# Kernel optimization log

Measured on AMD Instinct MI355X. Metric: run time of the kernel, lower is better.

Reference implementation:

```python
import jax, jax.numpy as jnp
import numpy as np

VOCAB = 100000; E = 256; H = 256; Hh = 128; K = 12
START = 9; STOP = 10; PAD = 11; NEG = -10000.0
B = 32; T = 512


def setup_inputs() -> dict:
    key = jax.random.key(0)
    ks = jax.random.split(key, 16)
    u = 1.0 / np.sqrt(Hh)  # pytorch LSTM init scale
    xav = lambda k, shape: jax.random.normal(k, shape, jnp.float32) * np.sqrt(2.0 / (shape[0] + shape[1]))
    trans = jax.random.normal(ks[10], (K, K), jnp.float32)
    trans = trans.at[START, :].set(NEG).at[:, STOP].set(NEG)
    trans = trans.at[PAD, :].set(NEG).at[:, PAD].set(NEG)
    return {
        "sentence": jax.random.randint(ks[0], (B, T), 0, VOCAB),
        "h0": jax.random.normal(ks[1], (2, B, Hh), jnp.float32),
        "c0": jax.random.normal(ks[2], (2, B, Hh), jnp.float32),
        "embed": xav(ks[3], (VOCAB, E)),
        "W_ih_f": jax.random.uniform(ks[4], (4 * Hh, E), jnp.float32, -u, u),
        "W_hh_f": jax.random.uniform(ks[5], (4 * Hh, Hh), jnp.float32, -u, u),
        "b_f": jax.random.uniform(ks[6], (4 * Hh,), jnp.float32, -u, u),
        "W_ih_r": jax.random.uniform(ks[7], (4 * Hh, E), jnp.float32, -u, u),
        "W_hh_r": jax.random.uniform(ks[8], (4 * Hh, Hh), jnp.float32, -u, u),
        "b_r": jax.random.uniform(ks[9], (4 * Hh,), jnp.float32, -u, u),
        "W_out": xav(ks[11], (K, H)),
        "b_out": jnp.zeros((K,), jnp.float32),
        "transitions": trans,
    }


def _lstm_dir(xe, W_ih, W_hh, b, h0, c0):
    # xe: [T,B,E]; precompute input contribution once (big GEMM outside scan)
    xg = jnp.einsum('tbe,ge->tbg', xe, W_ih) + b  # [T,B,4*Hh]
    def step(carry, xt):
        h, c = carry
        g = xt + h @ W_hh.T
        i, f, gg, o = jnp.split(g, 4, axis=-1)  # pytorch gate order i,f,g,o
        c = jax.nn.sigmoid(f) * c + jax.nn.sigmoid(i) * jnp.tanh(gg)
        h = jax.nn.sigmoid(o) * jnp.tanh(c)
        return (h, c), h
    _, hs = jax.lax.scan(step, (h0, c0), xg)
    return hs  # [T,B,Hh]


def reference(sentence, h0, c0, embed, W_ih_f, W_hh_f, b_f, W_ih_r, W_hh_r, b_r,
              W_out, b_out, transitions):
    xe = embed[sentence].transpose(1, 0, 2)  # [T,B,E]
    hs_f = _lstm_dir(xe, W_ih_f, W_hh_f, b_f, h0[0], c0[0])
    hs_r = _lstm_dir(xe[::-1], W_ih_r, W_hh_r, b_r, h0[1], c0[1])[::-1]
    hs = jnp.concatenate([hs_f, hs_r], axis=-1)           # [T,B,H]
    feats = hs @ W_out.T + b_out                          # [T,B,K]

    # Viterbi max-plus recurrence
    scores0 = jnp.full((B, K), NEG, jnp.float32).at[:, START].set(0.0)
    def vstep(scores, feat):
        m = scores[:, None, :] + transitions[None, :, :]  # [B,K_next,K_prev]
        ptr = jnp.argmax(m, axis=-1).astype(jnp.int32)
        return jnp.max(m, axis=-1) + feat, ptr
    scores, pointers = jax.lax.scan(vstep, scores0, feats)  # pointers [T,B,K]
    scores = scores + transitions[STOP]
    best_tag = jnp.argmax(scores, axis=-1).astype(jnp.int32)  # [B]

    # parallel backtrace (reverse scan, outputs in original time order)
    def back(tag, ptr):
        prev = jnp.take_along_axis(ptr, tag[:, None], axis=1)[:, 0]
        return prev, tag
    _, path = jax.lax.scan(back, best_tag, pointers, reverse=True)  # [T,B]
    return path.T  # [B,T] int32 best tag sequence
```

## Files before the change

### kernel.cpp

```cpp
#include <hip/hip_runtime.h>
#include <hip/hip_bf16.h>
#include <cmath>

#define TT 512
#define BB 32
#define EE 256
#define HH 128
#define KCRF 12
#define NEGF (-10000.0f)

__global__ __launch_bounds__(256) void k1_xg(const int* __restrict__ sent,
    const float* __restrict__ embed,
    const float* __restrict__ Wf, const float* __restrict__ bf,
    const float* __restrict__ Wr, const float* __restrict__ br,
    float* __restrict__ XG)
{
  __shared__ __align__(16) float As[64][36];
  __shared__ __align__(16) float Bs[128][36];
  const int tid = threadIdx.x;
  const int m0 = (blockIdx.x >> 3) * 64;
  const int n0 = (blockIdx.x & 7) * 128;
  const int ty = tid >> 4, tx = tid & 15;
  float acc[4][8];
#pragma unroll
  for (int i = 0; i < 4; ++i)
#pragma unroll
    for (int j = 0; j < 8; ++j) acc[i][j] = 0.f;

  for (int k0 = 0; k0 < 256; k0 += 32) {
#pragma unroll
    for (int r = 0; r < 2; ++r) {
      int idx = tid + r * 256;
      int row = idx >> 3;
      int c4 = (idx & 7) << 2;
      int R = m0 + row;
      int t = R >> 5, b = R & 31;
      const float4 v = *(const float4*)(embed + (long)sent[b * TT + t] * 256 + k0 + c4);
      *(float4*)&As[row][c4] = v;
    }
#pragma unroll
    for (int r = 0; r < 4; ++r) {
      int idx = tid + r * 256;
      int row = idx >> 3;
      int c4 = (idx & 7) << 2;
      int col = n0 + row;
      const float* src = (col < 512) ? (Wf + (long)col * 256) : (Wr + (long)(col - 512) * 256);
      const float4 v = *(const float4*)(src + k0 + c4);
      *(float4*)&Bs[row][c4] = v;
    }
    __syncthreads();
#pragma unroll
    for (int kk = 0; kk < 32; ++kk) {
      float a[4], bv[8];
#pragma unroll
      for (int i = 0; i < 4; ++i) a[i] = As[ty * 4 + i][kk];
#pragma unroll
      for (int j = 0; j < 8; ++j) bv[j] = Bs[tx + 16 * j][kk];
#pragma unroll
      for (int i = 0; i < 4; ++i)
#pragma unroll
        for (int j = 0; j < 8; ++j) acc[i][j] = fmaf(a[i], bv[j], acc[i][j]);
    }
    __syncthreads();
  }
#pragma unroll
  for (int i = 0; i < 4; ++i) {
    int R = m0 + ty * 4 + i;
#pragma unroll
    for (int j = 0; j < 8; ++j) {
      int col = n0 + tx + 16 * j;
      float bias = (col < 512) ? bf[col] : br[col - 512];
      XG[(long)R * 1024 + col] = acc[i][j] + bias;
    }
  }
}

__global__ __launch_bounds__(512) __attribute__((amdgpu_waves_per_eu(1)))
void k2_scan(const float* __restrict__ XG,
    const float* __restrict__ Whf, const float* __restrict__ Whr,
    const float* __restrict__ h0, const float* __restrict__ c0,
    float* __restrict__ HS)
{
  const int wg = blockIdx.x;
  const int dir = wg >> 5;
  const int b = wg & 31;
  const int j = threadIdx.x;
  const float* Wh = dir ? Whr : Whf;

  float4 w[32];
#pragma unroll
  for (int i = 0; i < 32; ++i)
    w[i] = *(const float4*)(Wh + (long)j * 128 + i * 4);

  __shared__ __align__(16) float hs[128];
  __shared__ float gs[512];
  float c = 0.f;
  if (j < 128) {
    hs[j] = h0[(dir * 32 + b) * 128 + j];
    c = c0[(dir * 32 + b) * 128 + j];
  }
  __syncthreads();

  const int t0 = dir ? (TT - 1) : 0;
  const long stepoff = dir ? -32768 : 32768;
  const float* xp = XG + ((long)t0 * 32 + b) * 1024 + dir * 512 + j;
  float xg_cur = *xp;
  const int gate = j >> 7;

  for (int s = 0; s < TT; ++s) {
    const int t = dir ? (TT - 1 - s) : s;
    float xg_nxt = 0.f;
    if (s + 1 < TT) { xp += stepoff; xg_nxt = *xp; }

    float a0 = xg_cur, a1 = 0.f, a2 = 0.f, a3 = 0.f;
#pragma unroll
    for (int i = 0; i < 32; ++i) {
      const float4 hv = *(const float4*)(hs + 4 * i);
      a0 = fmaf(w[i].x, hv.x, a0);
      a1 = fmaf(w[i].y, hv.y, a1);
      a2 = fmaf(w[i].z, hv.z, a2);
      a3 = fmaf(w[i].w, hv.w, a3);
    }
    const float acc = (a0 + a1) + (a2 + a3);
    const float act = (gate == 2) ? tanhf(acc) : (1.f / (1.f + expf(-acc)));
    gs[j] = act;
    __syncthreads();
    if (j < 128) {
      float ig = gs[j], fg = gs[128 + j], gg = gs[256 + j], og = gs[384 + j];
      c = fmaf(fg, c, ig * gg);
      float h = og * tanhf(c);
      hs[j] = h;
      HS[((long)t * 32 + b) * 256 + dir * 128 + j] = h;
    }
    __syncthreads();
    xg_cur = xg_nxt;
  }
}

__global__ __launch_bounds__(64) void k3_feats(const float* __restrict__ HS,
    const float* __restrict__ Wout, const float* __restrict__ bout,
    float* __restrict__ FE)
{
  __shared__ __align__(16) float ws[12 * 256];
  __shared__ float bs[12];
  const int tid = threadIdx.x;
  for (int i = tid; i < 768; i += 64)
    ((float4*)ws)[i] = ((const float4*)Wout)[i];
  if (tid < 12) bs[tid] = bout[tid];
  __syncthreads();
  const long row = (long)blockIdx.x * 64 + tid;
  const float4* hp = (const float4*)(HS + row * 256);
  float acc[12];
#pragma unroll
  for (int k = 0; k < 12; ++k) acc[k] = bs[k];
  for (int e4 = 0; e4 < 64; ++e4) {
    float4 hv = hp[e4];
#pragma unroll
    for (int k = 0; k < 12; ++k) {
      const float4 wv = *(const float4*)&ws[k * 256 + e4 * 4];
      acc[k] = fmaf(hv.x, wv.x, acc[k]);
      acc[k] = fmaf(hv.y, wv.y, acc[k]);
      acc[k] = fmaf(hv.z, wv.z, acc[k]);
      acc[k] = fmaf(hv.w, wv.w, acc[k]);
    }
  }
  const int t = (int)(row >> 5), b = (int)(row & 31);
#pragma unroll
  for (int k = 0; k < 12; ++k) FE[((long)t * 12 + k) * 32 + b] = acc[k];
}

__global__ __launch_bounds__(64) void k4_viterbi(const float* __restrict__ FE,
    const float* __restrict__ trans, int* __restrict__ out)
{
  __shared__ unsigned char ptrl[TT * 48];
  __shared__ __align__(16) float sc[2][4][12];
  const int l = threadIdx.x;
  const int bsub = l / 12;
  const int nxt = l % 12;
  const bool act = (bsub < 4);
  const int bs = act ? bsub : 0;
  const int b = blockIdx.x * 4 + bs;

  float tr[12], stopv[12];
#pragma unroll
  for (int p = 0; p < 12; ++p) tr[p] = trans[nxt * 12 + p];
#pragma unroll
  for (int p = 0; p < 12; ++p) stopv[p] = trans[10 * 12 + p];

  if (act) sc[0][bsub][nxt] = (nxt == 9) ? 0.f : NEGF;
  __syncthreads();

  float fnext = FE[nxt * 32 + b];
  for (int t = 0; t < TT; ++t) {
    const int cur = t & 1;
    const float feat = fnext;
    if (t + 1 < TT) fnext = FE[((t + 1) * 12 + nxt) * 32 + b];

    float sp[12];
    *(float4*)&sp[0] = *(const float4*)&sc[cur][bs][0];
    *(float4*)&sp[4] = *(const float4*)&sc[cur][bs][4];
    *(float4*)&sp[8] = *(const float4*)&sc[cur][bs][8];
    float best = -1e30f; int arg = 0;
#pragma unroll
    for (int p = 0; p < 12; ++p) {
      const float v = sp[p] + tr[p];
      if (v > best) { best = v; arg = p; }
    }
    if (act) {
      sc[cur ^ 1][bsub][nxt] = best + feat;
      ptrl[t * 48 + bsub * 12 + nxt] = (unsigned char)arg;
    }
    __syncthreads();
    }

  float best = -1e30f; int arg = 0;
#pragma unroll
  for (int p = 0; p < 12; ++p) {
    const float v = sc[0][bs][p] + stopv[p];
    if (v > best) { best = v; arg = p; }
  }
  if (act && nxt == 0) {
    int tag = arg;
    for (int t = TT - 1; t >= 0; --t) {
      out[b * TT + t] = tag;
      if (t) tag = ptrl[t * 48 + bsub * 12 + tag];
    }
  }
}

extern "C" void kernel_launch(void* const* d_in, const int* in_sizes, int n_in,
                              void* d_out, int out_size, void* d_ws, size_t ws_size,
                              hipStream_t stream)
{
  const int* sent = (const int*)d_in[0];
  const float* h0 = (const float*)d_in[1];
  const float* c0 = (const float*)d_in[2];
  const float* embed = (const float*)d_in[3];
  const float* Wif = (const float*)d_in[4];
  const float* Whf = (const float*)d_in[5];
  const float* bf = (const float*)d_in[6];
  const float* Wir = (const float*)d_in[7];
  const float* Whr = (const float*)d_in[8];
  const float* br = (const float*)d_in[9];
  const float* Wout = (const float*)d_in[10];
  const float* bout = (const float*)d_in[11];
  const float* trans = (const float*)d_in[12];

  char* ws = (char*)d_ws;
  float* XG = (float*)ws;
  float* HS = (float*)(ws + 67108864);
  float* FE = (float*)(ws + 67108864 + 16777216);
  int* out = (int*)d_out;

  hipLaunchKernelGGL(k1_xg, dim3(2048), dim3(256), 0, stream,
                     sent, embed, Wif, bf, Wir, br, XG);
  hipLaunchKernelGGL(k2_scan, dim3(64), dim3(512), 0, stream,
                     XG, Whf, Whr, h0, c0, HS);
  hipLaunchKernelGGL(k3_feats, dim3(256), dim3(64), 0, stream,
                     HS, Wout, bout, FE);
  hipLaunchKernelGGL(k4_viterbi, dim3(8), dim3(64), 0, stream,
                     FE, trans, out);
}
```

Measured before the change: 780.4 us.

## Fuse input-projection GEMM with LSTM scan using flag-based producer/consumer overlap

Merges the input-gate GEMM and the recurrent LSTM scan into one persistent kernel. 64 blocks run the scan while 192 blocks compute XG tiles in time order, outward from both ends so the forward and reverse directions are fed. The producers signal completion through atomic flags, and the scan blocks poll these flags every 16 steps. The goal is to hide the GEMM behind the serial scan, at the cost of requiring all blocks to be co-resident, a memset, and spin-wait overhead.

```diff
diff --git a/kernel.cpp b/kernel.cpp
--- a/kernel.cpp
+++ b/kernel.cpp
@@ -9,131 +9,154 @@
 #define KCRF 12
 #define NEGF (-10000.0f)
 
-__global__ __launch_bounds__(256) void k1_xg(const int* __restrict__ sent,
-    const float* __restrict__ embed,
-    const float* __restrict__ Wf, const float* __restrict__ bf,
-    const float* __restrict__ Wr, const float* __restrict__ br,
-    float* __restrict__ XG)
+__global__ __launch_bounds__(512)
+void k12_fused(const int* __restrict__ sent, const float* __restrict__ embed,
+               const float* __restrict__ Wf, const float* __restrict__ bfv,
+               const float* __restrict__ Wr, const float* __restrict__ brv,
+               const float* __restrict__ Whf, const float* __restrict__ Whr,
+               const float* __restrict__ h0, const float* __restrict__ c0,
+               float* XG, float* __restrict__ HS, int* flags)
 {
   __shared__ __align__(16) float As[64][36];
-  __shared__ __align__(16) float Bs[128][36];
-  const int tid = threadIdx.x;
-  const int m0 = (blockIdx.x >> 3) * 64;
-  const int n0 = (blockIdx.x & 7) * 128;
-  const int ty = tid >> 4, tx = tid & 15;
-  float acc[4][8];
-#pragma unroll
-  for (int i = 0; i < 4; ++i)
-#pragma unroll
-    for (int j = 0; j < 8; ++j) acc[i][j] = 0.f;
-
-  for (int k0 = 0; k0 < 256; k0 += 32) {
-#pragma unroll
-    for (int r = 0; r < 2; ++r) {
-      int idx = tid + r * 256;
-      int row = idx >> 3;
-      int c4 = (idx & 7) << 2;
-      int R = m0 + row;
-      int t = R >> 5, b = R & 31;
-      const float4 v = *(const float4*)(embed + (long)sent[b * TT + t] * 256 + k0 + c4);
-      *(float4*)&As[row][c4] = v;
-    }
-#pragma unroll
-    for (int r = 0; r < 4; ++r) {
-      int idx = tid + r * 256;
-      int row = idx >> 3;
-      int c4 = (idx & 7) << 2;
-      int col = n0 + row;
-      const float* src = (col < 512) ? (Wf + (long)col * 256) : (Wr + (long)(col - 512) * 256);
-      const float4 v = *(const float4*)(src + k0 + c4);
-      *(float4*)&Bs[row][c4] = v;
-    }
-    __syncthreads();
-#pragma unroll
-    for (int kk = 0; kk < 32; ++kk) {
-      float a[4], bv[8];
-#pragma unroll
-      for (int i = 0; i < 4; ++i) a[i] = As[ty * 4 + i][kk];
-#pragma unroll
-      for (int j = 0; j < 8; ++j) bv[j] = Bs[tx + 16 * j][kk];
-#pragma unroll
-      for (int i = 0; i < 4; ++i)
-#pragma unroll
-        for (int j = 0; j < 8; ++j) acc[i][j] = fmaf(a[i], bv[j], acc[i][j]);
-    }
-    __syncthreads();
-  }
-#pragma unroll
-  for (int i = 0; i < 4; ++i) {
-    int R = m0 + ty * 4 + i;
-#pragma unroll
-    for (int j = 0; j < 8; ++j) {
-      int col = n0 + tx + 16 * j;
-      float bias = (col < 512) ? bf[col] : br[col - 512];
-      XG[(long)R * 1024 + col] = acc[i][j] + bias;
-    }
-  }
-}
-
-__global__ __launch_bounds__(512) __attribute__((amdgpu_waves_per_eu(1)))
-void k2_scan(const float* __restrict__ XG,
-    const float* __restrict__ Whf, const float* __restrict__ Whr,
-    const float* __restrict__ h0, const float* __restrict__ c0,
-    float* __restrict__ HS)
-{
-  const int wg = blockIdx.x;
-  const int dir = wg >> 5;
-  const int b = wg & 31;
-  const int j = threadIdx.x;
-  const float* Wh = dir ? Whr : Whf;
-
-  float4 w[32];
-#pragma unroll
-  for (int i = 0; i < 32; ++i)
-    w[i] = *(const float4*)(Wh + (long)j * 128 + i * 4);
-
+  __shared__ __align__(16) float Bs[256][36];
   __shared__ __align__(16) float hs[128];
   __shared__ float gs[512];
-  float c = 0.f;
-  if (j < 128) {
-    hs[j] = h0[(dir * 32 + b) * 128 + j];
-    c = c0[(dir * 32 + b) * 128 + j];
-  }
-  __syncthreads();
-
-  const int t0 = dir ? (TT - 1) : 0;
-  const long stepoff = dir ? -32768 : 32768;
-  const float* xp = XG + ((long)t0 * 32 + b) * 1024 + dir * 512 + j;
-  float xg_cur = *xp;
-  const int gate = j >> 7;
-
-  for (int s = 0; s < TT; ++s) {
-    const int t = dir ? (TT - 1 - s) : s;
-    float xg_nxt = 0.f;
-    if (s + 1 < TT) { xp += stepoff; xg_nxt = *xp; }
-
-    float a0 = xg_cur, a1 = 0.f, a2 = 0.f, a3 = 0.f;
-#pragma unroll
-    for (int i = 0; i < 32; ++i) {
-      const float4 hv = *(const float4*)(hs + 4 * i);
-      a0 = fmaf(w[i].x, hv.x, a0);
-      a1 = fmaf(w[i].y, hv.y, a1);
-      a2 = fmaf(w[i].z, hv.z, a2);
-      a3 = fmaf(w[i].w, hv.w, a3);
-    }
-    const float acc = (a0 + a1) + (a2 + a3);
-    const float act = (gate == 2) ? tanhf(acc) : (1.f / (1.f + expf(-acc)));
-    gs[j] = act;
+
+  const int wg = blockIdx.x;
+  const int tid = threadIdx.x;
+
+  if (wg >= 64) {
+    const int sub = tid >> 8;
+    const int t256 = tid & 255;
+    const int ty = t256 >> 4, tx = t256 & 15;
+    for (int item = wg - 64; item < 1024; item += 192) {
+      const int g = item >> 2, q = item & 3;
+      const int pair = (q < 2) ? g : (255 - g);
+      const int half = q >> 1;
+      const int n0 = (q & 1) * 256 + half * 512;
+      const int m0 = pair * 64;
+      const int colbase = n0 + sub * 128;
+
+      float acc[4][8];
+#pragma unroll
+      for (int i = 0; i < 4; ++i)
+#pragma unroll
+        for (int j = 0; j < 8; ++j) acc[i][j] = 0.f;
+
+      for (int k0 = 0; k0 < 256; k0 += 32) {
+        {
+          int row = tid >> 3, c4 = (tid & 7) << 2;
+          int R = m0 + row, t = R >> 5, b = R & 31;
+          *(float4*)&As[row][c4] =
+              *(const float4*)(embed + (long)sent[b * TT + t] * 256 + k0 + c4);
+        }
+#pragma unroll
+        for (int r = 0; r < 4; ++r) {
+          int idx = tid + r * 512, row = idx >> 3, c4 = (idx & 7) << 2;
+          int col = n0 + row;
+          const float* src = (col < 512) ? (Wf + (long)col * 256)
+                                         : (Wr + (long)(col - 512) * 256);
+          *(float4*)&Bs[row][c4] = *(const float4*)(src + k0 + c4);
+        }
+        __syncthreads();
+#pragma unroll
+        for (int kk = 0; kk < 32; ++kk) {
+          float a[4], bv[8];
+#pragma unroll
+          for (int i = 0; i < 4; ++i) a[i] = As[ty * 4 + i][kk];
+#pragma unroll
+          for (int j = 0; j < 8; ++j) bv[j] = Bs[sub * 128 + tx + 16 * j][kk];
+#pragma unroll
+          for (int i = 0; i < 4; ++i)
+#pragma unroll
+            for (int j = 0; j < 8; ++j) acc[i][j] = fmaf(a[i], bv[j], acc[i][j]);
+        }
+        __syncthreads();
+      }
+#pragma unroll
+      for (int i = 0; i < 4; ++i) {
+        const long R = m0 + ty * 4 + i;
+#pragma unroll
+        for (int j = 0; j < 8; ++j) {
+          const int col = colbase + tx + 16 * j;
+          const float bias = (col < 512) ? bfv[col] : brv[col - 512];
+          XG[R * 1024 + col] = acc[i][j] + bias;
+        }
+      }
+      __syncthreads();
+      if (tid == 0) { __threadfence(); atomicAdd(&flags[pair * 2 + half], 1); }
+    }
+  } else {
+    const int dir = wg >> 5;
+    const int b = wg & 31;
+    const int j = tid;
+    const float* Wh = dir ? Whr : Whf;
+
+    float4 w[32];
+#pragma unroll
+    for (int i = 0; i < 32; ++i)
+      w[i] = *(const float4*)(Wh + (long)j * 128 + i * 4);
+
+    float c = 0.f;
+    if (j < 128) {
+      hs[j] = h0[(dir * 32 + b) * 128 + j];
+      c = c0[(dir * 32 + b) * 128 + j];
+    }
     __syncthreads();
-    if (j < 128) {
-      float ig = gs[j], fg = gs[128 + j], gg = gs[256 + j], og = gs[384 + j];
-      c = fmaf(fg, c, ig * gg);
-      float h = og * tanhf(c);
-      hs[j] = h;
-      HS[((long)t * 32 + b) * 256 + dir * 128 + j] = h;
-    }
-    __syncthreads();
-    xg_cur = xg_nxt;
+
+    const int t0 = dir ? (TT - 1) : 0;
+    const long stepoff = dir ? -32768 : 32768;
+    const float* xp = XG + ((long)t0 * 32 + b) * 1024 + dir * 512 + j;
+    const int gate = j >> 7;
+
+    {
+      if (tid < 9) {
+        int p0 = dir ? ((TT - 1) >> 1) : 0;
+        int p = dir ? (p0 - tid) : (p0 + tid);
+        p = p < 0 ? 0 : (p > 255 ? 255 : p);
+        while (atomicAdd(&flags[p * 2 + dir], 0) < 2) __builtin_amdgcn_s_sleep(8);
+      }
+      __syncthreads();
+    }
+    float xg_cur = *xp;
+
+    for (int s = 0; s < TT; ++s) {
+      if ((s & 15) == 0 && s) {
+        if (tid < 9) {
+          int p0 = (dir ? (TT - 1 - s) : s) >> 1;
+          int p = dir ? (p0 - tid) : (p0 + tid);
+          p = p < 0 ? 0 : (p > 255 ? 255 : p);
+          while (atomicAdd(&flags[p * 2 + dir], 0) < 2) __builtin_amdgcn_s_sleep(8);
+        }
+        __syncthreads();
+      }
+      const int t = dir ? (TT - 1 - s) : s;
+      float xg_nxt = 0.f;
+      if (s + 1 < TT) { xp += stepoff; xg_nxt = *xp; }
+
+      float a0 = xg_cur, a1 = 0.f, a2 = 0.f, a3 = 0.f;
+#pragma unroll
+      for (int i = 0; i < 32; ++i) {
+        const float4 hv = *(const float4*)(hs + 4 * i);
+        a0 = fmaf(w[i].x, hv.x, a0);
+        a1 = fmaf(w[i].y, hv.y, a1);
+        a2 = fmaf(w[i].z, hv.z, a2);
+        a3 = fmaf(w[i].w, hv.w, a3);
+      }
+      const float acc = (a0 + a1) + (a2 + a3);
+      const float act = (gate == 2) ? tanhf(acc) : (1.f / (1.f + expf(-acc)));
+      gs[j] = act;
+      __syncthreads();
+      if (j < 128) {
+        float ig = gs[j], fg = gs[128 + j], gg = gs[256 + j], og = gs[384 + j];
+        c = fmaf(fg, c, ig * gg);
+        float h = og * tanhf(c);
+        hs[j] = h;
+        HS[((long)t * 32 + b) * 256 + dir * 128 + j] = h;
+      }
+      __syncthreads();
+      xg_cur = xg_nxt;
+    }
   }
 }
 
@@ -211,7 +234,7 @@
       ptrl[t * 48 + bsub * 12 + nxt] = (unsigned char)arg;
     }
     __syncthreads();
-    }
+  }
 
   float best = -1e30f; int arg = 0;
 #pragma unroll
@@ -250,12 +273,14 @@
   float* XG = (float*)ws;
   float* HS = (float*)(ws + 67108864);
   float* FE = (float*)(ws + 67108864 + 16777216);
+  int* flags = (int*)(ws + 67108864 + 16777216 + 786432);
   int* out = (int*)d_out;
 
-  hipLaunchKernelGGL(k1_xg, dim3(2048), dim3(256), 0, stream,
-                     sent, embed, Wif, bf, Wir, br, XG);
-  hipLaunchKernelGGL(k2_scan, dim3(64), dim3(512), 0, stream,
-                     XG, Whf, Whr, h0, c0, HS);
+  hipMemsetAsync(flags, 0, 512 * sizeof(int), stream);
+
+  hipLaunchKernelGGL(k12_fused, dim3(256), dim3(512), 0, stream,
+                     sent, embed, Wif, bf, Wir, br, Whf, Whr, h0, c0,
+                     XG, HS, flags);
   hipLaunchKernelGGL(k3_feats, dim3(256), dim3(64), 0, stream,
                      HS, Wout, bout, FE);
   hipLaunchKernelGGL(k4_viterbi, dim3(8), dim3(64), 0, stream,
```

Result: slower. 811.3 us (+4.0%).
